# Kernel tuning notes

Hardware: AMD Instinct MI355X
Metric: run time of the kernel (lower is better)

Reference implementation:

```python
import jax, jax.numpy as jnp
import numpy as np

BATCH, NUM_HEADS, SEQ, HEAD_DIM = 2, 32, 2048, 128
QMAX = 127.0  # symmetric int8 quantization range


def _fake_quant(x):
    # per-(head, token) symmetric int8 quantization + dequantization
    scale = jnp.max(jnp.abs(x), axis=-1, keepdims=True) / QMAX
    scale = jnp.maximum(scale, jnp.asarray(1e-8, x.dtype))
    q = jnp.clip(jnp.round(x / scale), -QMAX, QMAX)  # packed int8 values
    return q * scale  # dequantized


def setup_inputs() -> dict:
    key = jax.random.key(0)
    kq, kk, kv = jax.random.split(key, 3)
    shape = (BATCH, NUM_HEADS, SEQ, HEAD_DIM)
    return {
        "query": jax.random.normal(kq, shape, dtype=jnp.float32),
        "key": jax.random.normal(kk, shape, dtype=jnp.float32),
        "value": jax.random.normal(kv, shape, dtype=jnp.float32),
    }


def reference(query, key, value):
    # quantize K/V on the fly into the cache, then attend over dequantized K/V
    k_dq = _fake_quant(key)
    v_dq = _fake_quant(value)
    scale = jnp.asarray(1.0 / np.sqrt(HEAD_DIM), query.dtype)
    logits = jnp.einsum("bhqd,bhkd->bhqk", query, k_dq) * scale  # [B,H,Sq,Sk]
    weights = jax.nn.softmax(logits, axis=-1)
    out = jnp.einsum("bhqk,bhkd->bhqd", weights, v_dq)
    return out
```

## Files before the change

### kernel.cpp

```cpp
#include <hip/hip_runtime.h>
#include <hip/hip_bf16.h>

#define B 2
#define H 32
#define S 2048
#define D 128
#define NT 32

typedef __bf16 bf16x8 __attribute__((ext_vector_type(8)));
typedef float f32x4 __attribute__((ext_vector_type(4)));

union BF8U { unsigned int u[4]; unsigned short s[8]; bf16x8 b; int4 i4; };

static constexpr float INV_SQRT_D = 0.08838834764831845f;
static constexpr float LOG2E = 1.4426950408889634f;
static constexpr float MFIX = 16.0f;
static constexpr int NROWS = B * H * S;

__device__ __forceinline__ unsigned short bfbits(float f) {
    union { __bf16 h; unsigned short s; } cv;
    cv.h = (__bf16)f;
    return cv.s;
}
__device__ __forceinline__ unsigned int pack2bf(float a, float b) {
    union { unsigned short s[2]; unsigned int u; } cv;
    cv.s[0] = bfbits(a); cv.s[1] = bfbits(b);
    return cv.u;
}
__device__ __forceinline__ float exp2_raw(float x) {
    float r;
    asm("v_exp_f32 %0, %1" : "=v"(r) : "v"(x));
    return r;
}

__global__ __launch_bounds__(256) void quant_k_kernel(
    const float* __restrict__ x, unsigned short* __restrict__ kpk,
    float* __restrict__ scl)
{
    const int row  = blockIdx.x * 4 + (threadIdx.x >> 6);
    const int lane = threadIdx.x & 63;
    const float2 v = *(const float2*)(x + (size_t)row * D + lane * 2);
    float m = fmaxf(fabsf(v.x), fabsf(v.y));
    #pragma unroll
    for (int off = 32; off; off >>= 1) m = fmaxf(m, __shfl_xor(m, off));
    const float scale = fmaxf(m / 127.0f, 1e-8f);
    const float q0 = fminf(fmaxf(rintf(v.x / scale), -127.0f), 127.0f);
    const float q1 = fminf(fmaxf(rintf(v.y / scale), -127.0f), 127.0f);
    const int bh = row >> 11, kv = row & 2047;
    const int t = kv >> 6, r = kv & 63, s = lane >> 2;
    unsigned short* dst = kpk + ((((size_t)bh * NT + t) * 16 + s) * 64 + r) * 8 + (lane & 3) * 2;
    *(unsigned int*)dst = pack2bf(q0, q1);
    if (lane == 0) scl[row] = scale * INV_SQRT_D * LOG2E;
}

__global__ __launch_bounds__(256) void quant_v_kernel(
    const float* __restrict__ x, unsigned short* __restrict__ vpk)
{
    __shared__ __align__(16) unsigned short vt[D][72];
    const int bh = blockIdx.y;
    const int t  = blockIdx.x;
    const int s0 = t * 64;
    const int tid = threadIdx.x;
    const int wave = tid >> 6, lane = tid & 63;

    #pragma unroll 1
    for (int i = 0; i < 16; i++) {
        const int tok = wave * 16 + i;
        const float2 v = *(const float2*)(x + ((size_t)bh * S + s0 + tok) * D + lane * 2);
        float m = fmaxf(fabsf(v.x), fabsf(v.y));
        #pragma unroll
        for (int off = 32; off; off >>= 1) m = fmaxf(m, __shfl_xor(m, off));
        const float scale = fmaxf(m / 127.0f, 1e-8f);
        const float q0 = fminf(fmaxf(rintf(v.x / scale), -127.0f), 127.0f);
        const float q1 = fminf(fmaxf(rintf(v.y / scale), -127.0f), 127.0f);
        vt[lane * 2    ][tok] = bfbits(q0 * scale);
        vt[lane * 2 + 1][tok] = bfbits(q1 * scale);
    }
    __syncthreads();
    const int d = tid & 127, sh = tid >> 7;
    const size_t tb = ((size_t)bh * NT + t) * 8192;
    #pragma unroll
    for (int p = 0; p < 4; p++) {
        const int s = p * 2 + sh, kk = s >> 2, gg = s & 3;
        BF8U o;
        *(unsigned long long*)&o.s[0] = *(const unsigned long long*)&vt[d][32 * kk + 4 * gg];
        *(unsigned long long*)&o.s[4] = *(const unsigned long long*)&vt[d][32 * kk + 16 + 4 * gg];
        *(int4*)(vpk + tb + ((size_t)s * 128 + d) * 8) = o.i4;
    }
}

__global__ __launch_bounds__(64, 2) void attn_kernel(
    const float* __restrict__ Q, const unsigned short* __restrict__ Kpk,
    const float* __restrict__ Ksc, const unsigned short* __restrict__ Vpk,
    float* __restrict__ Out)
{
    const int wg = blockIdx.x;
    const int swz = (wg & 7) * 512 + (wg >> 3);
    const int bh = swz >> 6;
    const int qt = swz & 63;
    const int lane = threadIdx.x & 63;
    const int g = lane >> 4, c = lane & 15;

    bf16x8 qfA[4], qfB[4];
    {
        const float* qpA = Q + ((size_t)bh * S + qt * 32 + c) * D + g * 8;
        const float* qpB = qpA + 16 * D;
        #pragma unroll
        for (int kk = 0; kk < 4; kk++) {
            float4 a = *(const float4*)(qpA + kk * 32);
            float4 b = *(const float4*)(qpA + kk * 32 + 4);
            BF8U t8;
            t8.s[0] = bfbits(a.x); t8.s[1] = bfbits(a.y); t8.s[2] = bfbits(a.z); t8.s[3] = bfbits(a.w);
            t8.s[4] = bfbits(b.x); t8.s[5] = bfbits(b.y); t8.s[6] = bfbits(b.z); t8.s[7] = bfbits(b.w);
            qfA[kk] = t8.b;
            a = *(const float4*)(qpB + kk * 32);
            b = *(const float4*)(qpB + kk * 32 + 4);
            t8.s[0] = bfbits(a.x); t8.s[1] = bfbits(a.y); t8.s[2] = bfbits(a.z); t8.s[3] = bfbits(a.w);
            t8.s[4] = bfbits(b.x); t8.s[5] = bfbits(b.y); t8.s[6] = bfbits(b.z); t8.s[7] = bfbits(b.w);
            qfB[kk] = t8.b;
        }
    }

    f32x4 accA[8], accB[8];
    const f32x4 zero = {0.f, 0.f, 0.f, 0.f};
    #pragma unroll
    for (int i = 0; i < 8; i++) { accA[i] = zero; accB[i] = zero; }
    float lA0 = 0.f, lA1 = 0.f, lB0 = 0.f, lB1 = 0.f;

    const unsigned short* kt = Kpk + (size_t)bh * NT * 8192;
    const unsigned short* vt = Vpk + (size_t)bh * NT * 8192;
    const float* kscp = Ksc + (size_t)bh * S;

    #pragma unroll 1
    for (int t = 0; t < NT; t++) {
        f32x4 sA[4], sB[4];
        __builtin_amdgcn_s_setprio(1);
        #pragma unroll
        for (int n = 0; n < 4; n++) {
            sA[n] = zero; sB[n] = zero;
            #pragma unroll
            for (int kk = 0; kk < 4; kk++) {
                bf16x8 kf = *(const bf16x8*)(kt + ((4 * kk + g) * 64 + n * 16 + c) * 8);
                sA[n] = __builtin_amdgcn_mfma_f32_16x16x32_bf16(kf, qfA[kk], sA[n], 0, 0, 0);
                sB[n] = __builtin_amdgcn_mfma_f32_16x16x32_bf16(kf, qfB[kk], sB[n], 0, 0, 0);
            }
        }
        __builtin_amdgcn_s_setprio(0);

        bf16x8 vf0[8];
        #pragma unroll
        for (int nd = 0; nd < 8; nd++)
            vf0[nd] = *(const bf16x8*)(vt + ((0 * 4 + g) * 128 + nd * 16 + c) * 8);

        #pragma unroll
        for (int n = 0; n < 4; n++) {
            const f32x4 ks4 = *(const f32x4*)(kscp + n * 16 + 4 * g);
            #pragma unroll
            for (int j = 0; j < 4; j++) {
                float p = exp2_raw(fmaf(sA[n][j], ks4[j], -MFIX));
                if (n & 1) lA1 += p; else lA0 += p;
                sA[n][j] = p;
                p = exp2_raw(fmaf(sB[n][j], ks4[j], -MFIX));
                if (n & 1) lB1 += p; else lB0 += p;
                sB[n][j] = p;
            }
        }

        {
            BF8U a8, b8;
            a8.u[0] = pack2bf(sA[0][0], sA[0][1]);
            a8.u[1] = pack2bf(sA[0][2], sA[0][3]);
            a8.u[2] = pack2bf(sA[1][0], sA[1][1]);
            a8.u[3] = pack2bf(sA[1][2], sA[1][3]);
            b8.u[0] = pack2bf(sB[0][0], sB[0][1]);
            b8.u[1] = pack2bf(sB[0][2], sB[0][3]);
            b8.u[2] = pack2bf(sB[1][0], sB[1][1]);
            b8.u[3] = pack2bf(sB[1][2], sB[1][3]);
            __builtin_amdgcn_s_setprio(1);
            #pragma unroll
            for (int nd = 0; nd < 8; nd++) {
                accA[nd] = __builtin_amdgcn_mfma_f32_16x16x32_bf16(a8.b, vf0[nd], accA[nd], 0, 0, 0);
                accB[nd] = __builtin_amdgcn_mfma_f32_16x16x32_bf16(b8.b, vf0[nd], accB[nd], 0, 0, 0);
            }
            __builtin_amdgcn_s_setprio(0);
        }

        bf16x8 vf1[8];
        #pragma unroll
        for (int nd = 0; nd < 8; nd++)
            vf1[nd] = *(const bf16x8*)(vt + ((1 * 4 + g) * 128 + nd * 16 + c) * 8);

        {
            BF8U a8, b8;
            a8.u[0] = pack2bf(sA[2][0], sA[2][1]);
            a8.u[1] = pack2bf(sA[2][2], sA[2][3]);
            a8.u[2] = pack2bf(sA[3][0], sA[3][1]);
            a8.u[3] = pack2bf(sA[3][2], sA[3][3]);
            b8.u[0] = pack2bf(sB[2][0], sB[2][1]);
            b8.u[1] = pack2bf(sB[2][2], sB[2][3]);
            b8.u[2] = pack2bf(sB[3][0], sB[3][1]);
            b8.u[3] = pack2bf(sB[3][2], sB[3][3]);
            __builtin_amdgcn_s_setprio(1);
            #pragma unroll
            for (int nd = 0; nd < 8; nd++) {
                accA[nd] = __builtin_amdgcn_mfma_f32_16x16x32_bf16(a8.b, vf1[nd], accA[nd], 0, 0, 0);
                accB[nd] = __builtin_amdgcn_mfma_f32_16x16x32_bf16(b8.b, vf1[nd], accB[nd], 0, 0, 0);
            }
            __builtin_amdgcn_s_setprio(0);
        }

        kt += 8192; vt += 8192; kscp += 64;
    }

    float lA = lA0 + lA1, lB = lB0 + lB1;
    lA += __shfl_xor(lA, 16);
    lA += __shfl_xor(lA, 32);
    lB += __shfl_xor(lB, 16);
    lB += __shfl_xor(lB, 32);
    const float invA = 1.0f / lA, invB = 1.0f / lB;
    float iqA[4], iqB[4];
    #pragma unroll
    for (int r = 0; r < 4; r++) {
        iqA[r] = __shfl(invA, 4 * g + r);
        iqB[r] = __shfl(invB, 4 * g + r);
    }
    const size_t obase = ((size_t)bh * S + qt * 32) * (size_t)D;
    #pragma unroll
    for (int r = 0; r < 4; r++) {
        const int q = 4 * g + r;
        #pragma unroll
        for (int nd = 0; nd < 8; nd++) {
            Out[obase + (size_t)q * D + nd * 16 + c] = accA[nd][r] * iqA[r];
            Out[obase + (size_t)(q + 16) * D + nd * 16 + c] = accB[nd][r] * iqB[r];
        }
    }
}

extern "C" void kernel_launch(void* const* d_in, const int* in_sizes, int n_in,
                              void* d_out, int out_size, void* d_ws, size_t ws_size,
                              hipStream_t stream) {
    const float* q = (const float*)d_in[0];
    const float* k = (const float*)d_in[1];
    const float* v = (const float*)d_in[2];
    float* out = (float*)d_out;

    const size_t ELEMS = (size_t)NROWS * D;
    unsigned short* kpk = (unsigned short*)d_ws;
    unsigned short* vpk = kpk + ELEMS;
    float* ks = (float*)(vpk + ELEMS);

    quant_k_kernel<<<NROWS / 4, 256, 0, stream>>>(k, kpk, ks);
    quant_v_kernel<<<dim3(NT, B * H), 256, 0, stream>>>(v, vpk);
    attn_kernel<<<4096, 64, 0, stream>>>(q, kpk, ks, vpk, out);
}
```

Before: 269.8 us.

## Software-pipeline K/V fragment loads across tiles and hoist scale loads

```diff
diff --git a/kernel.cpp b/kernel.cpp
--- a/kernel.cpp
+++ b/kernel.cpp
@@ -125,46 +125,82 @@
     const f32x4 zero = {0.f, 0.f, 0.f, 0.f};
     #pragma unroll
     for (int i = 0; i < 8; i++) { accA[i] = zero; accB[i] = zero; }
-    float lA0 = 0.f, lA1 = 0.f, lB0 = 0.f, lB1 = 0.f;
+    float lA = 0.f, lB = 0.f;
 
     const unsigned short* kt = Kpk + (size_t)bh * NT * 8192;
     const unsigned short* vt = Vpk + (size_t)bh * NT * 8192;
     const float* kscp = Ksc + (size_t)bh * S;
 
+    bf16x8 kf01[8];
+    #pragma unroll
+    for (int n = 0; n < 2; n++)
+        #pragma unroll
+        for (int kk = 0; kk < 4; kk++)
+            kf01[n * 4 + kk] = *(const bf16x8*)(kt + ((4 * kk + g) * 64 + n * 16 + c) * 8);
+
     #pragma unroll 1
     for (int t = 0; t < NT; t++) {
+        f32x4 ks4[4];
+        #pragma unroll
+        for (int n = 0; n < 4; n++) ks4[n] = *(const f32x4*)(kscp + n * 16 + 4 * g);
+
+        bf16x8 kf23[8];
+        #pragma unroll
+        for (int n = 0; n < 2; n++)
+            #pragma unroll
+            for (int kk = 0; kk < 4; kk++)
+                kf23[n * 4 + kk] = *(const bf16x8*)(kt + ((4 * kk + g) * 64 + (n + 2) * 16 + c) * 8);
+
+        bf16x8 vf0[8];
+        #pragma unroll
+        for (int nd = 0; nd < 8; nd++)
+            vf0[nd] = *(const bf16x8*)(vt + ((0 * 4 + g) * 128 + nd * 16 + c) * 8);
+
         f32x4 sA[4], sB[4];
         __builtin_amdgcn_s_setprio(1);
         #pragma unroll
+        for (int n = 0; n < 2; n++) {
+            sA[n] = zero; sB[n] = zero;
+            #pragma unroll
+            for (int kk = 0; kk < 4; kk++) {
+                sA[n] = __builtin_amdgcn_mfma_f32_16x16x32_bf16(kf01[n * 4 + kk], qfA[kk], sA[n], 0, 0, 0);
+                sB[n] = __builtin_amdgcn_mfma_f32_16x16x32_bf16(kf01[n * 4 + kk], qfB[kk], sB[n], 0, 0, 0);
+            }
+        }
+        #pragma unroll
+        for (int n = 0; n < 2; n++) {
+            sA[n + 2] = zero; sB[n + 2] = zero;
+            #pragma unroll
+            for (int kk = 0; kk < 4; kk++) {
+                sA[n + 2] = __builtin_amdgcn_mfma_f32_16x16x32_bf16(kf23[n * 4 + kk], qfA[kk], sA[n + 2], 0, 0, 0);
+                sB[n + 2] = __builtin_amdgcn_mfma_f32_16x16x32_bf16(kf23[n * 4 + kk], qfB[kk], sB[n + 2], 0, 0, 0);
+            }
+        }
+        __builtin_amdgcn_s_setprio(0);
+
+        #pragma unroll
         for (int n = 0; n < 4; n++) {
-            sA[n] = zero; sB[n] = zero;
-            #pragma unroll
-            for (int kk = 0; kk < 4; kk++) {
-                bf16x8 kf = *(const bf16x8*)(kt + ((4 * kk + g) * 64 + n * 16 + c) * 8);
-                sA[n] = __builtin_amdgcn_mfma_f32_16x16x32_bf16(kf, qfA[kk], sA[n], 0, 0, 0);
-                sB[n] = __builtin_amdgcn_mfma_f32_16x16x32_bf16(kf, qfB[kk], sB[n], 0, 0, 0);
-            }
-        }
-        __builtin_amdgcn_s_setprio(0);
-
-        bf16x8 vf0[8];
+            #pragma unroll
+            for (int j = 0; j < 4; j++) {
+                float p = exp2_raw(fmaf(sA[n][j], ks4[n][j], -MFIX));
+                lA += p;
+                sA[n][j] = p;
+                p = exp2_raw(fmaf(sB[n][j], ks4[n][j], -MFIX));
+                lB += p;
+                sB[n][j] = p;
+            }
+        }
+
+        #pragma unroll
+        for (int n = 0; n < 2; n++)
+            #pragma unroll
+            for (int kk = 0; kk < 4; kk++)
+                kf01[n * 4 + kk] = *(const bf16x8*)(kt + 8192 + ((4 * kk + g) * 64 + n * 16 + c) * 8);
+
+        bf16x8 vf1[8];
         #pragma unroll
         for (int nd = 0; nd < 8; nd++)
-            vf0[nd] = *(const bf16x8*)(vt + ((0 * 4 + g) * 128 + nd * 16 + c) * 8);
-
-        #pragma unroll
-        for (int n = 0; n < 4; n++) {
-            const f32x4 ks4 = *(const f32x4*)(kscp + n * 16 + 4 * g);
-            #pragma unroll
-            for (int j = 0; j < 4; j++) {
-                float p = exp2_raw(fmaf(sA[n][j], ks4[j], -MFIX));
-                if (n & 1) lA1 += p; else lA0 += p;
-                sA[n][j] = p;
-                p = exp2_raw(fmaf(sB[n][j], ks4[j], -MFIX));
-                if (n & 1) lB1 += p; else lB0 += p;
-                sB[n][j] = p;
-            }
-        }
+            vf1[nd] = *(const bf16x8*)(vt + ((1 * 4 + g) * 128 + nd * 16 + c) * 8);
 
         {
             BF8U a8, b8;
@@ -184,12 +220,6 @@
             }
             __builtin_amdgcn_s_setprio(0);
         }
-
-        bf16x8 vf1[8];
-        #pragma unroll
-        for (int nd = 0; nd < 8; nd++)
-            vf1[nd] = *(const bf16x8*)(vt + ((1 * 4 + g) * 128 + nd * 16 + c) * 8);
-
         {
             BF8U a8, b8;
             a8.u[0] = pack2bf(sA[2][0], sA[2][1]);
@@ -212,7 +242,6 @@
         kt += 8192; vt += 8192; kscp += 64;
     }
 
-    float lA = lA0 + lA1, lB = lB0 + lB1;
     lA += __shfl_xor(lA, 16);
     lA += __shfl_xor(lA, 32);
     lB += __shfl_xor(lB, 16);
```

After: 238.3 us, median of 2. 11.7% less time.
